# Optimization experiments

Measured on AMD Instinct MI355X. Metric: run time of the kernel, lower is better.

Reference implementation:

```python
import jax, jax.numpy as jnp
import numpy as np

A = -0.75  # torch bicubic coefficient
SCALES = [1.0, 0.9, 0.8, 0.7, 0.6]  # level=5
SOFTMAX_SCALE = 10.0
RES_SCALE = 1.0
ESCAPE_NAN = 1e-4


def _cubic_w(d):
    d = jnp.abs(d)
    return jnp.where(d <= 1.0, ((A + 2.0) * d - (A + 3.0)) * d * d + 1.0,
                     jnp.where(d < 2.0, ((A * d - 5.0 * A) * d + 8.0 * A) * d - 4.0 * A, 0.0))


def _resize_axis(x, out_size, axis):
    # bicubic, align_corners=True, 4-tap cubic conv with border clamp (matches torch)
    in_size = x.shape[axis]
    src = jnp.arange(out_size, dtype=jnp.float32) * (float(in_size - 1) / float(out_size - 1))
    i0 = jnp.floor(src).astype(jnp.int32)
    frac = src - i0.astype(jnp.float32)
    idx = jnp.clip(jnp.stack([i0 - 1, i0, i0 + 1, i0 + 2], 0), 0, in_size - 1)  # [4,out]
    w = jnp.stack([_cubic_w(frac + 1.0), _cubic_w(frac), _cubic_w(1.0 - frac), _cubic_w(2.0 - frac)], 0)  # [4,out]
    xm = jnp.moveaxis(x, axis, 0)
    g = xm[idx]  # [4,out,...]
    out = jnp.einsum('ko...,ko->o...', g, w)
    return jnp.moveaxis(out, 0, axis)


def bicubic_resize(x, oh, ow):
    return _resize_axis(_resize_axis(x, oh, 2), ow, 3)


def prelu(x, a):
    return jnp.where(x >= 0, x, a * x)


def conv1x1(x, W, b):
    # x [B,C,H,W], W [O,C], b [O]
    return jnp.einsum('oc,bchw->bohw', W, x) + b[None, :, None, None]


def extract_patches(x):
    # x [B,C,H,W] -> [B, H*W, C, 3, 3], 'same' padding, stride 1 (torch unfold order C,kh,kw)
    B, C, H, Wd = x.shape
    xp = jnp.pad(x, ((0, 0), (0, 0), (1, 1), (1, 1)))
    sl = [xp[:, :, dy:dy + H, dx:dx + Wd] for dy in range(3) for dx in range(3)]
    p = jnp.stack(sl, 0).reshape(3, 3, B, C, H, Wd)
    p = jnp.transpose(p, (2, 4, 5, 3, 0, 1))  # [B,H,W,C,3,3]
    return p.reshape(B, H * Wd, C, 3, 3)


def setup_inputs() -> dict:
    key = jax.random.key(0)
    ks = jax.random.split(key, 8)
    B, C, H, Wd = 2, 64, 64, 64
    Cm = 32
    return {
        'input': jax.random.normal(ks[0], (B, C, H, Wd), jnp.float32),
        'input_ref': jax.random.normal(ks[1], (B, C, H, Wd), jnp.float32),
        'Wb': jax.random.normal(ks[2], (Cm, C), jnp.float32) * 0.1,
        'bb': jax.random.normal(ks[3], (Cm,), jnp.float32) * 0.01,
        'Wm': jax.random.normal(ks[4], (Cm, C), jnp.float32) * 0.1,
        'bm': jax.random.normal(ks[5], (Cm,), jnp.float32) * 0.01,
        'Wa': jax.random.normal(ks[6], (C, C), jnp.float32) * 0.1,
        'ba': jax.random.normal(ks[7], (C,), jnp.float32) * 0.01,
        'a_prelu': jnp.full((1,), 0.25, jnp.float32),
    }


def reference(input, input_ref, Wb, bb, Wm, bm, Wa, ba, a_prelu):
    B, C, H, Wd = input.shape
    a = a_prelu[0]
    match_base = prelu(conv1x1(input, Wb, bb), a)  # [B,Cm,H,W]

    w_list, rw_list = [], []
    for s in SCALES:
        ref = input_ref if s == 1.0 else bicubic_resize(input_ref, int(H * s), int(Wd * s))
        base = prelu(conv1x1(ref, Wa, ba), a)   # conv_assembly
        rw_list.append(extract_patches(base))   # [B,Li,C,3,3]
        m = prelu(conv1x1(ref, Wm, bm), a)      # conv_match
        w_list.append(extract_patches(m))       # [B,Li,Cm,3,3]
    w = jnp.concatenate(w_list, axis=1)    # [B,L,Cm,3,3]
    rw = jnp.concatenate(rw_list, axis=1)  # [B,L,C,3,3]

    dn = ('NCHW', 'OIHW', 'NCHW')

    def per_sample(xi, wi, rwi):
        # xi [Cm,H,W]; wi [L,Cm,3,3]; rwi [L,C,3,3]
        nrm = jnp.maximum(jnp.sqrt(jnp.sum(wi * wi, axis=(1, 2, 3), keepdims=True)), ESCAPE_NAN)
        wn = wi / nrm
        scores = jax.lax.conv_general_dilated(xi[None], wn, (1, 1), [(1, 1), (1, 1)], dimension_numbers=dn)[0]  # [L,H,W]
        yi = jax.nn.softmax(scores * SOFTMAX_SCALE, axis=0)
        # conv_transpose2d(yi, rwi, stride=1, padding=1) == conv2d with flipped, transposed kernel, pad 1
        k = jnp.transpose(rwi, (1, 0, 2, 3))[:, :, ::-1, ::-1]  # [C,L,3,3]
        out = jax.lax.conv_general_dilated(yi[None], k, (1, 1), [(1, 1), (1, 1)], dimension_numbers=dn)[0] / 4.0
        return out  # [C,H,W]

    y = jax.vmap(per_sample)(match_base, w, rw)
    return y + input * RES_SCALE
```

## Files before the change

### kernel.cpp

```cpp
#include <hip/hip_runtime.h>
#include <stdint.h>


typedef __attribute__((ext_vector_type(8))) short bf16x8;
typedef __attribute__((ext_vector_type(4))) float f32x4;
typedef unsigned short ushort_t;

#define L_TOT  13326
#define NCHT   417
#define NPIX   4096
#define BCHUNK_E 9216
#define RCHUNK_E 18432
#define LOG2E10 14.4269504f
#define CT 256

__device__ __forceinline__ float cubw(float d) {
  d = fabsf(d);
  if (d <= 1.f) return (1.25f * d - 2.25f) * d * d + 1.f;
  if (d < 2.f)  return ((-0.75f * d + 3.75f) * d - 6.f) * d + 3.f;
  return 0.f;
}

__device__ __forceinline__ void decode_l(int l, int& S, int& off) {
  if (l < 4096)       { S = 64; off = 0; }
  else if (l < 7345)  { S = 57; off = 4096; }
  else if (l < 9946)  { S = 51; off = 7345; }
  else if (l < 11882) { S = 44; off = 9946; }
  else                { S = 38; off = 11882; }
}

__device__ __forceinline__ ushort_t f2bf(float f) {
  union { float f; uint32_t u; } v; v.f = f;
  uint32_t r = (v.u + 0x7fffu + ((v.u >> 16) & 1u)) >> 16;
  return (ushort_t)r;
}

__device__ __forceinline__ float preluf(float x, float a) { return x >= 0.f ? x : a * x; }

__device__ __forceinline__ void gll16(const ushort_t* g, ushort_t* l) {
  __builtin_amdgcn_global_load_lds(
      (const __attribute__((address_space(1))) unsigned int*)g,
      (__attribute__((address_space(3))) unsigned int*)l, 16, 0, 0);
}

__global__ void k_convref(const float* __restrict__ inref,
                          const float* __restrict__ Wm, const float* __restrict__ bm,
                          const float* __restrict__ Wa, const float* __restrict__ ba,
                          const float* __restrict__ ap,
                          float* __restrict__ mref, float* __restrict__ aref) {
  __shared__ float T[64][CT];
  __shared__ float Wy[CT][5], Wx[CT][5];
  __shared__ int   IY[CT], IX[CT];
  int blk = blockIdx.x;
  int oh = blk & 1; int lt = (blk >> 1) % 53; int b = blk / 106;
  int l0 = lt * CT;
  int tid = threadIdx.x;
  float a = ap[0];
  {
    int gl = l0 + tid;
    if (gl < L_TOT) {
      int S, off; decode_l(gl, S, off);
      int li = gl - off; int ly = li / S, lx = li % S;
      if (S == 64) {
        IY[tid] = -1; IX[tid] = ly * 64 + lx;
      } else {
        float sc = (float)(63.0 / (double)(S - 1));
        float sy = (float)ly * sc, sx = (float)lx * sc;
        int iy = (int)floorf(sy), ix = (int)floorf(sx);
        float fy = sy - (float)iy, fx = sx - (float)ix;
        IY[tid] = iy; IX[tid] = ix;
        Wy[tid][0] = cubw(fy + 1.f); Wy[tid][1] = cubw(fy);
        Wy[tid][2] = cubw(1.f - fy); Wy[tid][3] = cubw(2.f - fy);
        Wx[tid][0] = cubw(fx + 1.f); Wx[tid][1] = cubw(fx);
        Wx[tid][2] = cubw(1.f - fx); Wx[tid][3] = cubw(2.f - fx);
      }
    }
  }
  __syncthreads();
  for (int i = tid; i < 64 * CT; i += 256) {
    int c = i >> 8; int l2 = i & 255;
    int gl = l0 + l2;
    float val = 0.f;
    if (gl < L_TOT) {
      const float* img = inref + (size_t)(b * 64 + c) * 4096;
      int iy = IY[l2];
      if (iy == -1) {
        val = img[IX[l2]];
      } else {
        int ix = IX[l2];
        #pragma unroll
        for (int t = 0; t < 4; ++t) {
          int ty = iy - 1 + t; ty = ty < 0 ? 0 : (ty > 63 ? 63 : ty);
          float rv = 0.f;
          #pragma unroll
          for (int u = 0; u < 4; ++u) {
            int tx = ix - 1 + u; tx = tx < 0 ? 0 : (tx > 63 ? 63 : tx);
            rv += Wx[l2][u] * img[ty * 64 + tx];
          }
          val += Wy[l2][t] * rv;
        }
      }
    }
    T[c][l2] = val;
  }
  __syncthreads();
  int gl = l0 + tid;
  if (gl >= L_TOT) return;
  for (int oc = oh * 48; oc < oh * 48 + 48; ++oc) {
    const float* Wrow; float s;
    if (oc < 32) { Wrow = Wm + oc * 64; s = bm[oc]; }
    else         { Wrow = Wa + (oc - 32) * 64; s = ba[oc - 32]; }
    #pragma unroll 8
    for (int c = 0; c < 64; ++c) s += Wrow[c] * T[c][tid];
    s = preluf(s, a);
    if (oc < 32) mref[(size_t)(b * 32 + oc) * L_TOT + gl] = s;
    else         aref[(size_t)(b * 64 + oc - 32) * L_TOT + gl] = s;
  }
}

__global__ void k_mb(const float* __restrict__ input, const float* __restrict__ Wb,
                     const float* __restrict__ bb, const float* __restrict__ ap,
                     float* __restrict__ mbb, int n) {
  int idx = blockIdx.x * 256 + threadIdx.x;
  if (idx >= n) return;
  int p = idx % NPIX; int cm = (idx / NPIX) % 32; int b = idx / (32 * NPIX);
  float a = ap[0];
  float acc = bb[cm];
  for (int c = 0; c < 64; ++c) acc += Wb[cm * 64 + c] * input[(size_t)(b * 64 + c) * NPIX + p];
  mbb[(size_t)(b * 32 + cm) * NPIX + p] = preluf(acc, a);
}

__global__ void k_stage1(const float* __restrict__ mref, const float* __restrict__ mbb,
                         float* __restrict__ ssq, float* __restrict__ ssqA, int n) {
  int idx = blockIdx.x * 256 + threadIdx.x;
  if (idx >= n) return;
  if (idx < 2 * L_TOT) {
    int l = idx % L_TOT; int b = idx / L_TOT;
    float s = 0.f;
    for (int c = 0; c < 32; ++c) { float v = mref[(size_t)(b * 32 + c) * L_TOT + l]; s += v * v; }
    ssq[idx] = s;
  } else {
    int j = idx - 2 * L_TOT;
    int p = j % NPIX; int b = j / NPIX;
    float s = 0.f;
    for (int c = 0; c < 32; ++c) { float v = mbb[(size_t)(b * 32 + c) * NPIX + p]; s += v * v; }
    ssqA[j] = s;
  }
}

__global__ void k_stage2(const float* __restrict__ ssq, const float* __restrict__ ssqA,
                         float* __restrict__ invn, float* __restrict__ Mlog, int n) {
  int idx = blockIdx.x * 256 + threadIdx.x;
  if (idx >= n) return;
  if (idx < 2 * L_TOT) {
    int l = idx % L_TOT; int b = idx / L_TOT;
    int S, off; decode_l(l, S, off);
    int li = l - off; int ly = li / S, lx = li % S;
    float acc = 0.f;
    for (int dy = -1; dy <= 1; ++dy) {
      int ny = ly + dy; if (ny < 0 || ny >= S) continue;
      for (int dx = -1; dx <= 1; ++dx) {
        int nx = lx + dx; if (nx < 0 || nx >= S) continue;
        acc += ssq[(size_t)b * L_TOT + off + ny * S + nx];
      }
    }
    float nrm = sqrtf(acc); nrm = fmaxf(nrm, 1e-4f);
    invn[idx] = 1.f / nrm;
  } else {
    int j = idx - 2 * L_TOT;
    int p = j % NPIX; int b = j / NPIX;
    int y = p / 64, x = p % 64;
    float acc = 0.f;
    for (int dy = -1; dy <= 1; ++dy) {
      int ny = y + dy; if (ny < 0 || ny >= 64) continue;
      for (int dx = -1; dx <= 1; ++dx) {
        int nx = x + dx; if (nx < 0 || nx >= 64) continue;
        acc += ssqA[(size_t)b * NPIX + ny * 64 + nx];
      }
    }
    float qn = sqrtf(acc);
    float m = fmaxf(0.7f * qn, qn - 7.f);
    Mlog[j] = LOG2E10 * m;
  }
}

#define N_BS (2 * NCHT * 1152)
#define N_AIM (2 * NPIX * 36)
#define N_RS (2 * NCHT * 576 * 4)
__global__ void k_pack(const float* __restrict__ mref, const float* __restrict__ invn,
                       const float* __restrict__ mbb, const float* __restrict__ aref,
                       ushort_t* __restrict__ Bs, ushort_t* __restrict__ Am,
                       ushort_t* __restrict__ Rs, int n) {
  int idx = blockIdx.x * 256 + threadIdx.x;
  if (idx >= n) return;
  ushort_t v[8];
  if (idx < N_BS) {
    int segp = idx % 36; int col = (idx / 36) % 32;
    int ch = (idx / 1152) % NCHT; int b = idx / (1152 * NCHT);
    int segl = (segp & ~3) | ((segp & 3) ^ ((col >> 1) & 3));
    int l = ch * 32 + col;
    if (l < L_TOT) {
      int S, off; decode_l(l, S, off);
      int li = l - off; int ly = li / S, lx = li % S;
      float iv = invn[(size_t)b * L_TOT + l];
      #pragma unroll
      for (int e = 0; e < 8; ++e) {
        int k = segl * 8 + e;
        int c = k / 9; int r = k % 9; int dy = r / 3 - 1, dx = r % 3 - 1;
        int ny = ly + dy, nx = lx + dx;
        float val = 0.f;
        if (ny >= 0 && ny < S && nx >= 0 && nx < S)
          val = mref[(size_t)(b * 32 + c) * L_TOT + off + ny * S + nx] * iv;
        v[e] = f2bf(val);
      }
    } else {
      #pragma unroll
      for (int e = 0; e < 8; ++e) v[e] = 0;
    }
    *(uint4*)(Bs + ((size_t)(b * NCHT + ch) * BCHUNK_E + col * 288 + segp * 8)) = *(const uint4*)v;
  } else if (idx < N_BS + N_AIM) {
    int j = idx - N_BS;
    int k8 = j % 36; int p = (j / 36) % NPIX; int b = j / (36 * NPIX);
    int y = p / 64, x = p % 64;
    #pragma unroll
    for (int e = 0; e < 8; ++e) {
      int k = k8 * 8 + e;
      int c = k / 9; int r = k % 9; int dy = r / 3 - 1, dx = r % 3 - 1;
      int ny = y + dy, nx = x + dx;
      float val = 0.f;
      if (ny >= 0 && ny < 64 && nx >= 0 && nx < 64)
        val = mbb[(size_t)(b * 32 + c) * NPIX + ny * 64 + nx];
      v[e] = f2bf(val);
    }
    *(uint4*)(Am + ((size_t)(b * NPIX + p) * 288 + k8 * 8)) = *(const uint4*)v;
  } else {
    int j = idx - N_BS - N_AIM;
    int phys = j & 3; int q = j >> 2;
    int col = q % 576; q /= 576;
    int ch = q % NCHT; int b = q / NCHT;
    int c = col / 9; int r = col % 9; int dy = r / 3 - 1, dx = r % 3 - 1;
    int seg = phys ^ ((col >> 1) & 3);
    int lbase = ch * 32 + seg * 8;
    #pragma unroll
    for (int e = 0; e < 8; ++e) {
      int l = lbase + e;
      float val = 0.f;
      if (l < L_TOT) {
        int S, off; decode_l(l, S, off);
        int li = l - off; int ly = li / S, lx = li % S;
        int ny = ly + dy, nx = lx + dx;
        if (ny >= 0 && ny < S && nx >= 0 && nx < S)
          val = aref[(size_t)(b * 64 + c) * L_TOT + off + ny * S + nx];
      }
      v[e] = f2bf(val);
    }
    *(uint4*)(Rs + ((size_t)(b * NCHT + ch) * RCHUNK_E + col * 32 + phys * 8)) = *(const uint4*)v;
  }
}

__global__ __launch_bounds__(512, 2) void k_attn(const ushort_t* __restrict__ Am,
                                                 const ushort_t* __restrict__ Bs,
                                                 const ushort_t* __restrict__ Rs,
                                                 const float* __restrict__ Mlog,
                                                 float* __restrict__ Og,
                                                 float* __restrict__ Ol) {
  __shared__ ushort_t Rl[3][RCHUNK_E];
  __shared__ ushort_t Bl[2][BCHUNK_E];
  __shared__ ushort_t Pl[2][2048];
  int tid = threadIdx.x;
  int xcd = blockIdx.x & 7; int slot = blockIdx.x >> 3;
  int group = xcd >> 1;
  int spl = group & 1; int b = group >> 1;
  int tile = slot * 2 + (xcd & 1);
  int p0 = tile * 64;
  int wave = tid >> 6, lane = tid & 63, quad = lane >> 4, ln = lane & 15;
  int rbS = wave & 3, cbh = wave >> 2;
  int g = wave & 3, zrh = wave >> 2;
  int c0 = spl ? 209 : 0, c1 = spl ? NCHT : 209;

  bf16x8 af[9];
  {
    const ushort_t* arow = Am + (size_t)(b * NPIX + p0 + rbS * 16 + ln) * 288;
    #pragma unroll
    for (int kk = 0; kk < 9; ++kk) af[kk] = *(const bf16x8*)(arow + kk * 32 + quad * 8);
  }
  float mlg[4];
  #pragma unroll
  for (int r = 0; r < 4; ++r)
    mlg[r] = Mlog[(size_t)b * NPIX + p0 + rbS * 16 + quad * 4 + r];

  f32x4 acc[2][9];
  #pragma unroll
  for (int h = 0; h < 2; ++h)
    #pragma unroll
    for (int t = 0; t < 9; ++t) { acc[h][t][0] = acc[h][t][1] = acc[h][t][2] = acc[h][t][3] = 0.f; }
  float psum[4] = {0.f, 0.f, 0.f, 0.f};

  const ushort_t* RsB = Rs + (size_t)b * NCHT * RCHUNK_E + lane * 8;
  const ushort_t* BsB = Bs + (size_t)b * NCHT * BCHUNK_E + lane * 8;

  {
    const ushort_t* sB0 = BsB + (size_t)c0 * BCHUNK_E;
    ushort_t* dB0 = Bl[c0 & 1];
    #pragma unroll
    for (int u = wave; u < 18; u += 8) gll16(sB0 + u * 512, dB0 + u * 512);
    const ushort_t* sB1 = BsB + (size_t)(c0 + 1) * BCHUNK_E;
    ushort_t* dB1 = Bl[(c0 + 1) & 1];
    #pragma unroll
    for (int u = wave; u < 18; u += 8) gll16(sB1 + u * 512, dB1 + u * 512);
    const ushort_t* sR = RsB + (size_t)c0 * RCHUNK_E;
    ushort_t* dR = Rl[c0 % 3];
    #pragma unroll
    for (int u = wave; u < 36; u += 8) gll16(sR + u * 512, dR + u * 512);
  }
  __syncthreads();

  int col32 = cbh * 16 + ln;
  int bswz = (col32 >> 1) & 3;
  int rpar = c0 % 3;
  for (int ch = c0; ch < c1; ++ch) {
    int par = ch & 1;
    int rnext = rpar == 2 ? 0 : rpar + 1;
    f32x4 sa, sb;
    sa[0] = sa[1] = sa[2] = sa[3] = 0.f;
    sb[0] = sb[1] = sb[2] = sb[3] = 0.f;
    #pragma unroll
    for (int kk = 0; kk < 9; ++kk) {
      int segp = kk * 4 + (quad ^ bswz);
      bf16x8 bf = *(const bf16x8*)&Bl[par][col32 * 288 + segp * 8];
      if (kk == 4 || kk == 5 || kk == 6 || kk == 7)
        sb = __builtin_amdgcn_mfma_f32_16x16x32_bf16(af[kk], bf, sb, 0, 0, 0);
      else
        sa = __builtin_amdgcn_mfma_f32_16x16x32_bf16(af[kk], bf, sa, 0, 0, 0);
    }
    int colw = ch * 32 + col32;
    bool valid = colw < L_TOT;
    #pragma unroll
    for (int r = 0; r < 4; ++r) {
      float sv = sa[r] + sb[r];
      float pv = valid ? exp2f(fmaf(sv, LOG2E10, -mlg[r])) : 0.f;
      int row = rbS * 16 + quad * 4 + r;
      int seg = cbh * 2 + (ln >> 3);
      int swz = seg ^ ((row >> 1) & 3);
      Pl[par][row * 32 + swz * 8 + (ln & 7)] = f2bf(pv);
      psum[r] += pv;
    }
    __syncthreads();
    if (ch + 2 < c1) {
      const ushort_t* sB = BsB + (size_t)(ch + 2) * BCHUNK_E;
      ushort_t* dB = Bl[par];
      #pragma unroll
      for (int u = wave; u < 18; u += 8) gll16(sB + u * 512, dB + u * 512);
    }
    if (ch + 1 < c1) {
      const ushort_t* sR = RsB + (size_t)(ch + 1) * RCHUNK_E;
      ushort_t* dR = Rl[rnext];
      #pragma unroll
      for (int u = wave; u < 36; u += 8) gll16(sR + u * 512, dR + u * 512);
    }
    bf16x8 pf0, pf1;
    {
      int sw = quad ^ ((ln >> 1) & 3);
      pf0 = *(const bf16x8*)&Pl[par][(zrh * 32 + ln) * 32 + sw * 8];
      pf1 = *(const bf16x8*)&Pl[par][(zrh * 32 + 16 + ln) * 32 + sw * 8];
    }
    #pragma unroll
    for (int t = 0; t < 9; ++t) {
      int col = g * 144 + t * 16 + ln;
      int swz = quad ^ ((col >> 1) & 3);
      bf16x8 rf = *(const bf16x8*)&Rl[rpar][col * 32 + swz * 8];
      acc[0][t] = __builtin_amdgcn_mfma_f32_16x16x32_bf16(pf0, rf, acc[0][t], 0, 0, 0);
      acc[1][t] = __builtin_amdgcn_mfma_f32_16x16x32_bf16(pf1, rf, acc[1][t], 0, 0, 0);
    }
    rpar = rnext;
  }

  #pragma unroll
  for (int m = 1; m <= 8; m <<= 1)
    #pragma unroll
    for (int r = 0; r < 4; ++r) psum[r] += __shfl_xor(psum[r], m);
  int sb2 = spl * 2 + b;
  if (ln == 0) {
    #pragma unroll
    for (int r = 0; r < 4; ++r) {
      int row = p0 + rbS * 16 + quad * 4 + r;
      Ol[(size_t)(sb2 * 2 + cbh) * NPIX + row] = psum[r];
    }
  }
  #pragma unroll
  for (int h = 0; h < 2; ++h)
    #pragma unroll
    for (int t = 0; t < 9; ++t) {
      int colg = g * 144 + t * 16 + ln;
      #pragma unroll
      for (int r = 0; r < 4; ++r) {
        int row = p0 + zrh * 32 + h * 16 + quad * 4 + r;
        Og[((size_t)sb2 * NPIX + row) * 576 + colg] = acc[h][t][r];
      }
    }
}

__global__ void k_inv(const float* __restrict__ Ol, float* __restrict__ inv, int n) {
  int idx = blockIdx.x * 256 + threadIdx.x;
  if (idx >= n) return;
  int b = idx / NPIX; int p = idx % NPIX;
  float s = 0.f;
  #pragma unroll
  for (int spl = 0; spl < 2; ++spl)
    #pragma unroll
    for (int cbh = 0; cbh < 2; ++cbh)
      s += Ol[(size_t)(((spl * 2 + b) * 2) + cbh) * NPIX + p];
  inv[idx] = 1.f / s;
}

__global__ void k_final(const float* __restrict__ Og, const float* __restrict__ inv,
                        const float* __restrict__ input, float* __restrict__ out) {
  __shared__ float T[32][65];
  int blk = blockIdx.x;
  int xh = blk & 1; int y = (blk >> 1) & 63; int b = blk >> 7;
  int tid = threadIdx.x;
  const size_t S1 = (size_t)2 * NPIX * 576;
  for (int it = 0; it < 8; ++it) {
    int lin = it * 256 + tid;
    int c = lin & 63, x32 = lin >> 6;
    int x = xh * 32 + x32;
    float acc = 0.f;
    for (int j = 0; j < 3; ++j) {
      int qy = y + 1 - j; if (qy < 0 || qy >= 64) continue;
      for (int i2 = 0; i2 < 3; ++i2) {
        int qx = x + 1 - i2; if (qx < 0 || qx >= 64) continue;
        int p = qy * 64 + qx;
        size_t e = ((size_t)b * NPIX + p) * 576 + c * 9 + j * 3 + i2;
        acc += (Og[e] + Og[e + S1]) * inv[b * NPIX + p];
      }
    }
    T[x32][c] = acc;
  }
  __syncthreads();
  for (int it = 0; it < 8; ++it) {
    int lin = it * 256 + tid;
    int x32 = lin & 31, c = lin >> 5;
    int o = ((b * 64 + c) * 64 + y) * 64 + xh * 32 + x32;
    out[o] = 0.25f * T[x32][c] + input[o];
  }
}

extern "C" void kernel_launch(void* const* d_in, const int* in_sizes, int n_in,
                              void* d_out, int out_size, void* d_ws, size_t ws_size,
                              hipStream_t stream) {
  (void)in_sizes; (void)n_in; (void)out_size; (void)ws_size;
  const float* input = (const float*)d_in[0];
  const float* inref = (const float*)d_in[1];
  const float* Wb = (const float*)d_in[2];
  const float* bb = (const float*)d_in[3];
  const float* Wm = (const float*)d_in[4];
  const float* bm = (const float*)d_in[5];
  const float* Wa = (const float*)d_in[6];
  const float* ba = (const float*)d_in[7];
  const float* ap = (const float*)d_in[8];
  float* out = (float*)d_out;

  char* ws = (char*)d_ws;
  size_t off = 0;
  auto alloc = [&](size_t bytes) -> char* {
    char* p = ws + off; off = (off + bytes + 255) & ~(size_t)255; return p;
  };
  ushort_t* Am   = (ushort_t*)alloc((size_t)2 * NPIX * 288 * 2);
  ushort_t* Bs   = (ushort_t*)alloc((size_t)2 * NCHT * BCHUNK_E * 2);
  ushort_t* Rs   = (ushort_t*)alloc((size_t)2 * NCHT * RCHUNK_E * 2);
  float*    Ol   = (float*)alloc((size_t)8 * NPIX * 4);
  float*    inv  = (float*)alloc((size_t)2 * NPIX * 4);
  float*    Mlog = (float*)alloc((size_t)2 * NPIX * 4);
  float*    ssqA = (float*)alloc((size_t)2 * NPIX * 4);
  size_t og_bytes = (size_t)4 * NPIX * 576 * 4;
  char* big = alloc(og_bytes);
  float* Og = (float*)big;
  size_t eoff = 0;
  auto ealloc = [&](size_t bytes) -> char* {
    char* p = big + eoff; eoff = (eoff + bytes + 255) & ~(size_t)255; return p;
  };
  float* mref = (float*)ealloc((size_t)2 * 32 * L_TOT * 4);
  float* aref = (float*)ealloc((size_t)2 * 64 * L_TOT * 4);
  float* mbb  = (float*)ealloc((size_t)2 * 32 * NPIX * 4);
  float* ssq  = (float*)ealloc((size_t)2 * L_TOT * 4);
  float* invn = (float*)ealloc((size_t)2 * L_TOT * 4);

  k_convref<<<212, 256, 0, stream>>>(inref, Wm, bm, Wa, ba, ap, mref, aref);
  int n3 = 2 * 32 * NPIX;
  k_mb<<<(n3 + 255) / 256, 256, 0, stream>>>(input, Wb, bb, ap, mbb, n3);
  int ns = 2 * L_TOT + 2 * NPIX;
  k_stage1<<<(ns + 255) / 256, 256, 0, stream>>>(mref, mbb, ssq, ssqA, ns);
  k_stage2<<<(ns + 255) / 256, 256, 0, stream>>>(ssq, ssqA, invn, Mlog, ns);
  int np = N_BS + N_AIM + N_RS;
  k_pack<<<(np + 255) / 256, 256, 0, stream>>>(mref, invn, mbb, aref, Bs, Am, Rs, np);

  k_attn<<<256, 512, 0, stream>>>(Am, Bs, Rs, Mlog, Og, Ol);
  k_inv<<<(2 * NPIX + 255) / 256, 256, 0, stream>>>(Ol, inv, 2 * NPIX);
  k_final<<<256, 256, 0, stream>>>(Og, inv, input, out);
}
```

Measured before the change: 470.4 us.

## Specialize waves into score/softmax producers and PV consumers pipelined by chunk

The attention kernel now splits its eight waves into two roles. Waves 0-3 compute the QK scores and exp-probabilities for chunk ch, each covering two 16-row tiles. Waves 4-7 run the P·R MFMA accumulation for chunk ch-1, each covering all 64 rows, with the accumulator and the A fragments sharing one register array. This lets the softmax/exp phase of one chunk overlap the value accumulation of the previous chunk, and the R staging drops from three LDS buffers to two. The risks are load imbalance between the two roles, high register use per wave, and fewer waves available to hide latency in each phase.

```diff
diff --git a/kernel.cpp b/kernel.cpp
--- a/kernel.cpp
+++ b/kernel.cpp
@@ -264,7 +264,7 @@
                                                  const float* __restrict__ Mlog,
                                                  float* __restrict__ Og,
                                                  float* __restrict__ Ol) {
-  __shared__ ushort_t Rl[3][RCHUNK_E];
+  __shared__ ushort_t Rl[2][RCHUNK_E];
   __shared__ ushort_t Bl[2][BCHUNK_E];
   __shared__ ushort_t Pl[2][2048];
   int tid = threadIdx.x;
@@ -274,130 +274,140 @@
   int tile = slot * 2 + (xcd & 1);
   int p0 = tile * 64;
   int wave = tid >> 6, lane = tid & 63, quad = lane >> 4, ln = lane & 15;
-  int rbS = wave & 3, cbh = wave >> 2;
-  int g = wave & 3, zrh = wave >> 2;
+  bool isS = wave < 4;
+  int rbp = wave & 1, cbh = (wave >> 1) & 1;
+  int g = wave & 3;
   int c0 = spl ? 209 : 0, c1 = spl ? NCHT : 209;
 
-  bf16x8 af[9];
-  {
-    const ushort_t* arow = Am + (size_t)(b * NPIX + p0 + rbS * 16 + ln) * 288;
-    #pragma unroll
-    for (int kk = 0; kk < 9; ++kk) af[kk] = *(const bf16x8*)(arow + kk * 32 + quad * 8);
-  }
-  float mlg[4];
-  #pragma unroll
-  for (int r = 0; r < 4; ++r)
-    mlg[r] = Mlog[(size_t)b * NPIX + p0 + rbS * 16 + quad * 4 + r];
-
-  f32x4 acc[2][9];
-  #pragma unroll
-  for (int h = 0; h < 2; ++h)
-    #pragma unroll
-    for (int t = 0; t < 9; ++t) { acc[h][t][0] = acc[h][t][1] = acc[h][t][2] = acc[h][t][3] = 0.f; }
-  float psum[4] = {0.f, 0.f, 0.f, 0.f};
+  f32x4 st[36];
+  float mlg[2][4], psum[2][4];
+
+  if (isS) {
+    #pragma unroll
+    for (int h = 0; h < 2; ++h) {
+      const ushort_t* arow = Am + (size_t)(b * NPIX + p0 + (rbp + 2 * h) * 16 + ln) * 288;
+      #pragma unroll
+      for (int kk = 0; kk < 9; ++kk)
+        st[h * 9 + kk] = __builtin_bit_cast(f32x4, *(const bf16x8*)(arow + kk * 32 + quad * 8));
+      #pragma unroll
+      for (int r = 0; r < 4; ++r) {
+        mlg[h][r] = Mlog[(size_t)b * NPIX + p0 + (rbp + 2 * h) * 16 + quad * 4 + r];
+        psum[h][r] = 0.f;
+      }
+    }
+  } else {
+    #pragma unroll
+    for (int i = 0; i < 36; ++i) { st[i][0] = 0.f; st[i][1] = 0.f; st[i][2] = 0.f; st[i][3] = 0.f; }
+  }
 
   const ushort_t* RsB = Rs + (size_t)b * NCHT * RCHUNK_E + lane * 8;
   const ushort_t* BsB = Bs + (size_t)b * NCHT * BCHUNK_E + lane * 8;
 
-  {
-    const ushort_t* sB0 = BsB + (size_t)c0 * BCHUNK_E;
-    ushort_t* dB0 = Bl[c0 & 1];
-    #pragma unroll
-    for (int u = wave; u < 18; u += 8) gll16(sB0 + u * 512, dB0 + u * 512);
-    const ushort_t* sB1 = BsB + (size_t)(c0 + 1) * BCHUNK_E;
-    ushort_t* dB1 = Bl[(c0 + 1) & 1];
-    #pragma unroll
-    for (int u = wave; u < 18; u += 8) gll16(sB1 + u * 512, dB1 + u * 512);
-    const ushort_t* sR = RsB + (size_t)c0 * RCHUNK_E;
-    ushort_t* dR = Rl[c0 % 3];
-    #pragma unroll
-    for (int u = wave; u < 36; u += 8) gll16(sR + u * 512, dR + u * 512);
-  }
-  __syncthreads();
+  auto stageB = [&](int chunk, int sl) {
+    const ushort_t* s = BsB + (size_t)chunk * BCHUNK_E;
+    ushort_t* d = Bl[sl];
+    #pragma unroll
+    for (int u = wave; u < 18; u += 8) gll16(s + u * 512, d + u * 512);
+  };
+  auto stageR = [&](int chunk, int sl) {
+    const ushort_t* s = RsB + (size_t)chunk * RCHUNK_E;
+    ushort_t* d = Rl[sl];
+    #pragma unroll
+    for (int u = wave; u < 36; u += 8) gll16(s + u * 512, d + u * 512);
+  };
 
   int col32 = cbh * 16 + ln;
   int bswz = (col32 >> 1) & 3;
-  int rpar = c0 % 3;
-  for (int ch = c0; ch < c1; ++ch) {
-    int par = ch & 1;
-    int rnext = rpar == 2 ? 0 : rpar + 1;
-    f32x4 sa, sb;
-    sa[0] = sa[1] = sa[2] = sa[3] = 0.f;
-    sb[0] = sb[1] = sb[2] = sb[3] = 0.f;
-    #pragma unroll
-    for (int kk = 0; kk < 9; ++kk) {
-      int segp = kk * 4 + (quad ^ bswz);
-      bf16x8 bf = *(const bf16x8*)&Bl[par][col32 * 288 + segp * 8];
-      if (kk == 4 || kk == 5 || kk == 6 || kk == 7)
-        sb = __builtin_amdgcn_mfma_f32_16x16x32_bf16(af[kk], bf, sb, 0, 0, 0);
-      else
-        sa = __builtin_amdgcn_mfma_f32_16x16x32_bf16(af[kk], bf, sa, 0, 0, 0);
-    }
-    int colw = ch * 32 + col32;
-    bool valid = colw < L_TOT;
-    #pragma unroll
-    for (int r = 0; r < 4; ++r) {
-      float sv = sa[r] + sb[r];
-      float pv = valid ? exp2f(fmaf(sv, LOG2E10, -mlg[r])) : 0.f;
-      int row = rbS * 16 + quad * 4 + r;
-      int seg = cbh * 2 + (ln >> 3);
-      int swz = seg ^ ((row >> 1) & 3);
-      Pl[par][row * 32 + swz * 8 + (ln & 7)] = f2bf(pv);
-      psum[r] += pv;
-    }
-    __syncthreads();
-    if (ch + 2 < c1) {
-      const ushort_t* sB = BsB + (size_t)(ch + 2) * BCHUNK_E;
-      ushort_t* dB = Bl[par];
-      #pragma unroll
-      for (int u = wave; u < 18; u += 8) gll16(sB + u * 512, dB + u * 512);
-    }
-    if (ch + 1 < c1) {
-      const ushort_t* sR = RsB + (size_t)(ch + 1) * RCHUNK_E;
-      ushort_t* dR = Rl[rnext];
-      #pragma unroll
-      for (int u = wave; u < 36; u += 8) gll16(sR + u * 512, dR + u * 512);
-    }
-    bf16x8 pf0, pf1;
-    {
-      int sw = quad ^ ((ln >> 1) & 3);
-      pf0 = *(const bf16x8*)&Pl[par][(zrh * 32 + ln) * 32 + sw * 8];
-      pf1 = *(const bf16x8*)&Pl[par][(zrh * 32 + 16 + ln) * 32 + sw * 8];
-    }
+  int psw = quad ^ ((ln >> 1) & 3);
+
+  auto zstep = [&](int parz) {
+    bf16x8 pf[4];
+    #pragma unroll
+    for (int j = 0; j < 4; ++j)
+      pf[j] = *(const bf16x8*)&Pl[parz][(j * 16 + ln) * 32 + psw * 8];
     #pragma unroll
     for (int t = 0; t < 9; ++t) {
       int col = g * 144 + t * 16 + ln;
       int swz = quad ^ ((col >> 1) & 3);
-      bf16x8 rf = *(const bf16x8*)&Rl[rpar][col * 32 + swz * 8];
-      acc[0][t] = __builtin_amdgcn_mfma_f32_16x16x32_bf16(pf0, rf, acc[0][t], 0, 0, 0);
-      acc[1][t] = __builtin_amdgcn_mfma_f32_16x16x32_bf16(pf1, rf, acc[1][t], 0, 0, 0);
-    }
-    rpar = rnext;
-  }
-
-  #pragma unroll
-  for (int m = 1; m <= 8; m <<= 1)
-    #pragma unroll
-    for (int r = 0; r < 4; ++r) psum[r] += __shfl_xor(psum[r], m);
-  int sb2 = spl * 2 + b;
-  if (ln == 0) {
-    #pragma unroll
-    for (int r = 0; r < 4; ++r) {
-      int row = p0 + rbS * 16 + quad * 4 + r;
-      Ol[(size_t)(sb2 * 2 + cbh) * NPIX + row] = psum[r];
-    }
-  }
-  #pragma unroll
-  for (int h = 0; h < 2; ++h)
-    #pragma unroll
-    for (int t = 0; t < 9; ++t) {
-      int colg = g * 144 + t * 16 + ln;
-      #pragma unroll
-      for (int r = 0; r < 4; ++r) {
-        int row = p0 + zrh * 32 + h * 16 + quad * 4 + r;
-        Og[((size_t)sb2 * NPIX + row) * 576 + colg] = acc[h][t][r];
-      }
-    }
+      bf16x8 rf = *(const bf16x8*)&Rl[parz][col * 32 + swz * 8];
+      #pragma unroll
+      for (int j = 0; j < 4; ++j)
+        st[j * 9 + t] = __builtin_amdgcn_mfma_f32_16x16x32_bf16(pf[j], rf, st[j * 9 + t], 0, 0, 0);
+    }
+  };
+
+  stageB(c0, c0 & 1);
+  stageB(c0 + 1, (c0 + 1) & 1);
+  stageR(c0, c0 & 1);
+  __syncthreads();
+
+  for (int ch = c0; ch < c1; ++ch) {
+    int par = ch & 1;
+    if (isS) {
+      f32x4 s0, s1;
+      s0[0] = s0[1] = s0[2] = s0[3] = 0.f;
+      s1[0] = s1[1] = s1[2] = s1[3] = 0.f;
+      #pragma unroll
+      for (int kk = 0; kk < 9; ++kk) {
+        int segp = kk * 4 + (quad ^ bswz);
+        bf16x8 bfrag = *(const bf16x8*)&Bl[par][col32 * 288 + segp * 8];
+        s0 = __builtin_amdgcn_mfma_f32_16x16x32_bf16(__builtin_bit_cast(bf16x8, st[kk]), bfrag, s0, 0, 0, 0);
+        s1 = __builtin_amdgcn_mfma_f32_16x16x32_bf16(__builtin_bit_cast(bf16x8, st[9 + kk]), bfrag, s1, 0, 0, 0);
+      }
+      int colw = ch * 32 + col32;
+      bool valid = colw < L_TOT;
+      #pragma unroll
+      for (int h = 0; h < 2; ++h)
+        #pragma unroll
+        for (int r = 0; r < 4; ++r) {
+          float sv = h ? s1[r] : s0[r];
+          float pv = valid ? exp2f(fmaf(sv, LOG2E10, -mlg[h][r])) : 0.f;
+          int row = (rbp + 2 * h) * 16 + quad * 4 + r;
+          int seg = cbh * 2 + (ln >> 3);
+          int swz = seg ^ ((row >> 1) & 3);
+          Pl[par][row * 32 + swz * 8 + (ln & 7)] = f2bf(pv);
+          psum[h][r] += pv;
+        }
+    } else if (ch > c0) {
+      zstep(par ^ 1);
+    }
+    __syncthreads();
+    if (ch + 2 < c1) stageB(ch + 2, par);
+    if (ch + 1 < c1) stageR(ch + 1, par ^ 1);
+  }
+
+  if (isS) {
+    #pragma unroll
+    for (int m = 1; m <= 8; m <<= 1)
+      #pragma unroll
+      for (int h = 0; h < 2; ++h)
+        #pragma unroll
+        for (int r = 0; r < 4; ++r) psum[h][r] += __shfl_xor(psum[h][r], m);
+    int sb2 = spl * 2 + b;
+    if (ln == 0) {
+      #pragma unroll
+      for (int h = 0; h < 2; ++h)
+        #pragma unroll
+        for (int r = 0; r < 4; ++r) {
+          int row = p0 + (rbp + 2 * h) * 16 + quad * 4 + r;
+          Ol[(size_t)(sb2 * 2 + cbh) * NPIX + row] = psum[h][r];
+        }
+    }
+  } else {
+    zstep((c1 - 1) & 1);
+    int sb2 = spl * 2 + b;
+    #pragma unroll
+    for (int j = 0; j < 4; ++j)
+      #pragma unroll
+      for (int t = 0; t < 9; ++t) {
+        int colg = g * 144 + t * 16 + ln;
+        #pragma unroll
+        for (int r = 0; r < 4; ++r) {
+          int row = p0 + j * 16 + quad * 4 + r;
+          Og[((size_t)sb2 * NPIX + row) * 576 + colg] = st[j * 9 + t][r];
+        }
+      }
+  }
 }
 
 __global__ void k_inv(const float* __restrict__ Ol, float* __restrict__ inv, int n) {
```

New measurement: 500.5 us. 1.06x slower.

## Software-pipeline score and aggregation MFMAs across chunks with partial vmcnt waits

Applied to the files above, without the earlier changes.

Restructures the main chunk loop so the score MFMAs for chunk ch are interleaved with the aggregation MFMAs for chunk ch-1, using a prologue and an epilogue. Full __syncthreads is replaced by an s_waitcnt vmcnt(4) plus s_barrier, so in-flight prefetches of the next chunk are not drained at every iteration. R is now staged two chunks ahead in its triple buffer. The intent is to overlap the exp/softmax dependency chain and the global loads with MFMA work and to remove a barrier per chunk. The hand-counted vmcnt value is fragile if the number of loads issued per wave changes.

```diff
diff --git a/kernel.cpp b/kernel.cpp
--- a/kernel.cpp
+++ b/kernel.cpp
@@ -299,39 +299,44 @@
   const ushort_t* RsB = Rs + (size_t)b * NCHT * RCHUNK_E + lane * 8;
   const ushort_t* BsB = Bs + (size_t)b * NCHT * BCHUNK_E + lane * 8;
 
-  {
-    const ushort_t* sB0 = BsB + (size_t)c0 * BCHUNK_E;
-    ushort_t* dB0 = Bl[c0 & 1];
-    #pragma unroll
-    for (int u = wave; u < 18; u += 8) gll16(sB0 + u * 512, dB0 + u * 512);
-    const ushort_t* sB1 = BsB + (size_t)(c0 + 1) * BCHUNK_E;
-    ushort_t* dB1 = Bl[(c0 + 1) & 1];
-    #pragma unroll
-    for (int u = wave; u < 18; u += 8) gll16(sB1 + u * 512, dB1 + u * 512);
-    const ushort_t* sR = RsB + (size_t)c0 * RCHUNK_E;
-    ushort_t* dR = Rl[c0 % 3];
-    #pragma unroll
-    for (int u = wave; u < 36; u += 8) gll16(sR + u * 512, dR + u * 512);
-  }
-  __syncthreads();
+  auto stageB = [&](int chunk, int sl) {
+    const ushort_t* s = BsB + (size_t)chunk * BCHUNK_E;
+    ushort_t* d = Bl[sl];
+    #pragma unroll
+    for (int u = wave; u < 18; u += 8) gll16(s + u * 512, d + u * 512);
+  };
+  auto stageR = [&](int chunk, int sl) {
+    const ushort_t* s = RsB + (size_t)chunk * RCHUNK_E;
+    ushort_t* d = Rl[sl];
+    #pragma unroll
+    for (int u = wave; u < 36; u += 8) gll16(s + u * 512, d + u * 512);
+  };
 
   int col32 = cbh * 16 + ln;
   int bswz = (col32 >> 1) & 3;
-  int rpar = c0 % 3;
-  for (int ch = c0; ch < c1; ++ch) {
-    int par = ch & 1;
-    int rnext = rpar == 2 ? 0 : rpar + 1;
+  int psw = quad ^ ((ln >> 1) & 3);
+
+  stageB(c0, c0 & 1);
+  stageB(c0 + 1, (c0 + 1) & 1);
+  stageR(c0, c0 % 3);
+  stageR(c0 + 1, (c0 + 1) % 3);
+  __syncthreads();
+
+  int rz = c0 % 3;
+
+  {
+    int ch = c0, par = ch & 1;
     f32x4 sa, sb;
     sa[0] = sa[1] = sa[2] = sa[3] = 0.f;
     sb[0] = sb[1] = sb[2] = sb[3] = 0.f;
     #pragma unroll
     for (int kk = 0; kk < 9; ++kk) {
       int segp = kk * 4 + (quad ^ bswz);
-      bf16x8 bf = *(const bf16x8*)&Bl[par][col32 * 288 + segp * 8];
-      if (kk == 4 || kk == 5 || kk == 6 || kk == 7)
-        sb = __builtin_amdgcn_mfma_f32_16x16x32_bf16(af[kk], bf, sb, 0, 0, 0);
+      bf16x8 bfrag = *(const bf16x8*)&Bl[par][col32 * 288 + segp * 8];
+      if (kk >= 4 && kk <= 7)
+        sb = __builtin_amdgcn_mfma_f32_16x16x32_bf16(af[kk], bfrag, sb, 0, 0, 0);
       else
-        sa = __builtin_amdgcn_mfma_f32_16x16x32_bf16(af[kk], bf, sa, 0, 0, 0);
+        sa = __builtin_amdgcn_mfma_f32_16x16x32_bf16(af[kk], bfrag, sa, 0, 0, 0);
     }
     int colw = ch * 32 + col32;
     bool valid = colw < L_TOT;
@@ -345,34 +350,69 @@
       Pl[par][row * 32 + swz * 8 + (ln & 7)] = f2bf(pv);
       psum[r] += pv;
     }
-    __syncthreads();
+    asm volatile("s_waitcnt vmcnt(4) lgkmcnt(0)\n\ts_barrier" ::: "memory");
     if (ch + 2 < c1) {
-      const ushort_t* sB = BsB + (size_t)(ch + 2) * BCHUNK_E;
-      ushort_t* dB = Bl[par];
-      #pragma unroll
-      for (int u = wave; u < 18; u += 8) gll16(sB + u * 512, dB + u * 512);
-    }
-    if (ch + 1 < c1) {
-      const ushort_t* sR = RsB + (size_t)(ch + 1) * RCHUNK_E;
-      ushort_t* dR = Rl[rnext];
-      #pragma unroll
-      for (int u = wave; u < 36; u += 8) gll16(sR + u * 512, dR + u * 512);
-    }
-    bf16x8 pf0, pf1;
-    {
-      int sw = quad ^ ((ln >> 1) & 3);
-      pf0 = *(const bf16x8*)&Pl[par][(zrh * 32 + ln) * 32 + sw * 8];
-      pf1 = *(const bf16x8*)&Pl[par][(zrh * 32 + 16 + ln) * 32 + sw * 8];
-    }
+      stageB(ch + 2, par);
+      int s2 = rz + 2; if (s2 >= 3) s2 -= 3;
+      stageR(ch + 2, s2);
+    }
+  }
+
+  for (int ch = c0 + 1; ch < c1; ++ch) {
+    int par = ch & 1;
+    bf16x8 pf0 = *(const bf16x8*)&Pl[par ^ 1][(zrh * 32 + ln) * 32 + psw * 8];
+    bf16x8 pf1 = *(const bf16x8*)&Pl[par ^ 1][(zrh * 32 + 16 + ln) * 32 + psw * 8];
+    f32x4 sa, sb;
+    sa[0] = sa[1] = sa[2] = sa[3] = 0.f;
+    sb[0] = sb[1] = sb[2] = sb[3] = 0.f;
+    #pragma unroll
+    for (int kk = 0; kk < 9; ++kk) {
+      int segp = kk * 4 + (quad ^ bswz);
+      bf16x8 bfrag = *(const bf16x8*)&Bl[par][col32 * 288 + segp * 8];
+      if (kk >= 4 && kk <= 7)
+        sb = __builtin_amdgcn_mfma_f32_16x16x32_bf16(af[kk], bfrag, sb, 0, 0, 0);
+      else
+        sa = __builtin_amdgcn_mfma_f32_16x16x32_bf16(af[kk], bfrag, sa, 0, 0, 0);
+      int col = g * 144 + kk * 16 + ln;
+      int swz = quad ^ ((col >> 1) & 3);
+      bf16x8 rf = *(const bf16x8*)&Rl[rz][col * 32 + swz * 8];
+      acc[0][kk] = __builtin_amdgcn_mfma_f32_16x16x32_bf16(pf0, rf, acc[0][kk], 0, 0, 0);
+      acc[1][kk] = __builtin_amdgcn_mfma_f32_16x16x32_bf16(pf1, rf, acc[1][kk], 0, 0, 0);
+    }
+    int colw = ch * 32 + col32;
+    bool valid = colw < L_TOT;
+    #pragma unroll
+    for (int r = 0; r < 4; ++r) {
+      float sv = sa[r] + sb[r];
+      float pv = valid ? exp2f(fmaf(sv, LOG2E10, -mlg[r])) : 0.f;
+      int row = rbS * 16 + quad * 4 + r;
+      int seg = cbh * 2 + (ln >> 3);
+      int swz = seg ^ ((row >> 1) & 3);
+      Pl[par][row * 32 + swz * 8 + (ln & 7)] = f2bf(pv);
+      psum[r] += pv;
+    }
+    asm volatile("s_waitcnt vmcnt(4) lgkmcnt(0)\n\ts_barrier" ::: "memory");
+    if (ch + 2 < c1) {
+      stageB(ch + 2, par);
+      stageR(ch + 2, rz);
+    }
+    rz = rz == 2 ? 0 : rz + 1;
+  }
+
+  asm volatile("s_waitcnt vmcnt(0)\n\ts_barrier" ::: "memory");
+
+  {
+    int parz = (c1 - 1) & 1;
+    bf16x8 pf0 = *(const bf16x8*)&Pl[parz][(zrh * 32 + ln) * 32 + psw * 8];
+    bf16x8 pf1 = *(const bf16x8*)&Pl[parz][(zrh * 32 + 16 + ln) * 32 + psw * 8];
     #pragma unroll
     for (int t = 0; t < 9; ++t) {
       int col = g * 144 + t * 16 + ln;
       int swz = quad ^ ((col >> 1) & 3);
-      bf16x8 rf = *(const bf16x8*)&Rl[rpar][col * 32 + swz * 8];
+      bf16x8 rf = *(const bf16x8*)&Rl[rz][col * 32 + swz * 8];
       acc[0][t] = __builtin_amdgcn_mfma_f32_16x16x32_bf16(pf0, rf, acc[0][t], 0, 0, 0);
       acc[1][t] = __builtin_amdgcn_mfma_f32_16x16x32_bf16(pf1, rf, acc[1][t], 0, 0, 0);
     }
-    rpar = rnext;
   }
 
   #pragma unroll
```

Result: slower. 512.8 us (+9.0%).

## Add 128-row attention tile variant with four-way key split

Applied to the files above, without the earlier changes.

Adds k_attn128, which processes 128 query pixels per block instead of 64, splitting the key chunks four ways across XCD groups rather than two. Each staged B/R chunk in shared memory is reused by twice as many query rows, which halves global and LDS traffic per FLOP. R staging drops from triple to double buffering to fit LDS. The cost is more accumulator registers, a larger partial-output buffer, and more partial sums for k_final to reduce. The new path is chosen at runtime only if the workspace is large enough, otherwise the old kernel runs.

```diff
diff --git a/kernel.cpp b/kernel.cpp
--- a/kernel.cpp
+++ b/kernel.cpp
@@ -258,12 +258,12 @@
   }
 }
 
-__global__ __launch_bounds__(512, 2) void k_attn(const ushort_t* __restrict__ Am,
-                                                 const ushort_t* __restrict__ Bs,
-                                                 const ushort_t* __restrict__ Rs,
-                                                 const float* __restrict__ Mlog,
-                                                 float* __restrict__ Og,
-                                                 float* __restrict__ Ol) {
+__global__ __launch_bounds__(512, 2) void k_attn64(const ushort_t* __restrict__ Am,
+                                                   const ushort_t* __restrict__ Bs,
+                                                   const ushort_t* __restrict__ Rs,
+                                                   const float* __restrict__ Mlog,
+                                                   float* __restrict__ Og,
+                                                   float* __restrict__ Ol) {
   __shared__ ushort_t Rl[3][RCHUNK_E];
   __shared__ ushort_t Bl[2][BCHUNK_E];
   __shared__ ushort_t Pl[2][2048];
@@ -400,13 +400,148 @@
     }
 }
 
-__global__ void k_inv(const float* __restrict__ Ol, float* __restrict__ inv, int n) {
+__global__ __launch_bounds__(512, 2) void k_attn128(const ushort_t* __restrict__ Am,
+                                                    const ushort_t* __restrict__ Bs,
+                                                    const ushort_t* __restrict__ Rs,
+                                                    const float* __restrict__ Mlog,
+                                                    float* __restrict__ Og,
+                                                    float* __restrict__ Ol) {
+  __shared__ ushort_t Rl[2][RCHUNK_E];
+  __shared__ ushort_t Bl[2][BCHUNK_E];
+  __shared__ ushort_t Pl[2][4096];
+  int tid = threadIdx.x;
+  int xcd = blockIdx.x & 7; int slot = blockIdx.x >> 3;
+  int spl = xcd >> 1; int b = xcd & 1;
+  int p0 = slot * 128;
+  int wave = tid >> 6, lane = tid & 63, quad = lane >> 4, ln = lane & 15;
+  int rbq = wave & 3, cb = wave >> 2;
+  int g = wave & 3, zrh = wave >> 2;
+  int c0 = (spl * NCHT) >> 2;
+  int c1 = ((spl + 1) * NCHT) >> 2;
+
+  bf16x8 af[2][9];
+  float mlg[2][4], psum[2][4];
+  #pragma unroll
+  for (int h = 0; h < 2; ++h) {
+    const ushort_t* arow = Am + (size_t)(b * NPIX + p0 + (rbq + 4 * h) * 16 + ln) * 288;
+    #pragma unroll
+    for (int kk = 0; kk < 9; ++kk) af[h][kk] = *(const bf16x8*)(arow + kk * 32 + quad * 8);
+    #pragma unroll
+    for (int r = 0; r < 4; ++r) {
+      mlg[h][r] = Mlog[(size_t)b * NPIX + p0 + (rbq + 4 * h) * 16 + quad * 4 + r];
+      psum[h][r] = 0.f;
+    }
+  }
+  f32x4 acc[4][9];
+  #pragma unroll
+  for (int j = 0; j < 4; ++j)
+    #pragma unroll
+    for (int t = 0; t < 9; ++t) { acc[j][t][0] = acc[j][t][1] = acc[j][t][2] = acc[j][t][3] = 0.f; }
+
+  const ushort_t* RsB = Rs + (size_t)b * NCHT * RCHUNK_E + lane * 8;
+  const ushort_t* BsB = Bs + (size_t)b * NCHT * BCHUNK_E + lane * 8;
+
+  auto stageB = [&](int chunk, int sl) {
+    const ushort_t* s = BsB + (size_t)chunk * BCHUNK_E;
+    ushort_t* d = Bl[sl];
+    #pragma unroll
+    for (int u = wave; u < 18; u += 8) gll16(s + u * 512, d + u * 512);
+  };
+  auto stageR = [&](int chunk, int sl) {
+    const ushort_t* s = RsB + (size_t)chunk * RCHUNK_E;
+    ushort_t* d = Rl[sl];
+    #pragma unroll
+    for (int u = wave; u < 36; u += 8) gll16(s + u * 512, d + u * 512);
+  };
+
+  int col32 = cb * 16 + ln;
+  int bswz = (col32 >> 1) & 3;
+  int psw = quad ^ ((ln >> 1) & 3);
+
+  stageB(c0, c0 & 1);
+  stageB(c0 + 1, (c0 + 1) & 1);
+  stageR(c0, c0 & 1);
+  __syncthreads();
+
+  for (int ch = c0; ch < c1; ++ch) {
+    int par = ch & 1;
+    f32x4 s0, s1;
+    s0[0] = s0[1] = s0[2] = s0[3] = 0.f;
+    s1[0] = s1[1] = s1[2] = s1[3] = 0.f;
+    #pragma unroll
+    for (int kk = 0; kk < 9; ++kk) {
+      int segp = kk * 4 + (quad ^ bswz);
+      bf16x8 bfrag = *(const bf16x8*)&Bl[par][col32 * 288 + segp * 8];
+      s0 = __builtin_amdgcn_mfma_f32_16x16x32_bf16(af[0][kk], bfrag, s0, 0, 0, 0);
+      s1 = __builtin_amdgcn_mfma_f32_16x16x32_bf16(af[1][kk], bfrag, s1, 0, 0, 0);
+    }
+    int colw = ch * 32 + col32;
+    bool valid = colw < L_TOT;
+    #pragma unroll
+    for (int h = 0; h < 2; ++h)
+      #pragma unroll
+      for (int r = 0; r < 4; ++r) {
+        float sv = h ? s1[r] : s0[r];
+        float pv = valid ? exp2f(fmaf(sv, LOG2E10, -mlg[h][r])) : 0.f;
+        int row = (rbq + 4 * h) * 16 + quad * 4 + r;
+        int seg = cb * 2 + (ln >> 3);
+        int swz = seg ^ ((row >> 1) & 3);
+        Pl[par][row * 32 + swz * 8 + (ln & 7)] = f2bf(pv);
+        psum[h][r] += pv;
+      }
+    __syncthreads();
+    if (ch + 2 < c1) stageB(ch + 2, par);
+    if (ch + 1 < c1) stageR(ch + 1, par ^ 1);
+    bf16x8 pf[4];
+    #pragma unroll
+    for (int j = 0; j < 4; ++j)
+      pf[j] = *(const bf16x8*)&Pl[par][(zrh * 64 + j * 16 + ln) * 32 + psw * 8];
+    #pragma unroll
+    for (int t = 0; t < 9; ++t) {
+      int col = g * 144 + t * 16 + ln;
+      int swz = quad ^ ((col >> 1) & 3);
+      bf16x8 rf = *(const bf16x8*)&Rl[par][col * 32 + swz * 8];
+      #pragma unroll
+      for (int j = 0; j < 4; ++j)
+        acc[j][t] = __builtin_amdgcn_mfma_f32_16x16x32_bf16(pf[j], rf, acc[j][t], 0, 0, 0);
+    }
+  }
+
+  #pragma unroll
+  for (int m = 1; m <= 8; m <<= 1)
+    #pragma unroll
+    for (int h = 0; h < 2; ++h)
+      #pragma unroll
+      for (int r = 0; r < 4; ++r) psum[h][r] += __shfl_xor(psum[h][r], m);
+  int sb2 = spl * 2 + b;
+  if (ln == 0) {
+    #pragma unroll
+    for (int h = 0; h < 2; ++h)
+      #pragma unroll
+      for (int r = 0; r < 4; ++r) {
+        int row = p0 + (rbq + 4 * h) * 16 + quad * 4 + r;
+        Ol[(size_t)(sb2 * 2 + cb) * NPIX + row] = psum[h][r];
+      }
+  }
+  #pragma unroll
+  for (int j = 0; j < 4; ++j)
+    #pragma unroll
+    for (int t = 0; t < 9; ++t) {
+      int colg = g * 144 + t * 16 + ln;
+      #pragma unroll
+      for (int r = 0; r < 4; ++r) {
+        int row = p0 + zrh * 64 + j * 16 + quad * 4 + r;
+        Og[((size_t)sb2 * NPIX + row) * 576 + colg] = acc[j][t][r];
+      }
+    }
+}
+
+__global__ void k_inv(const float* __restrict__ Ol, float* __restrict__ inv, int n, int nspl) {
   int idx = blockIdx.x * 256 + threadIdx.x;
   if (idx >= n) return;
   int b = idx / NPIX; int p = idx % NPIX;
   float s = 0.f;
-  #pragma unroll
-  for (int spl = 0; spl < 2; ++spl)
+  for (int spl = 0; spl < nspl; ++spl)
     #pragma unroll
     for (int cbh = 0; cbh < 2; ++cbh)
       s += Ol[(size_t)(((spl * 2 + b) * 2) + cbh) * NPIX + p];
@@ -414,7 +549,7 @@
 }
 
 __global__ void k_final(const float* __restrict__ Og, const float* __restrict__ inv,
-                        const float* __restrict__ input, float* __restrict__ out) {
+                        const float* __restrict__ input, float* __restrict__ out, int nsl) {
   __shared__ float T[32][65];
   int blk = blockIdx.x;
   int xh = blk & 1; int y = (blk >> 1) & 63; int b = blk >> 7;
@@ -431,7 +566,9 @@
         int qx = x + 1 - i2; if (qx < 0 || qx >= 64) continue;
         int p = qy * 64 + qx;
         size_t e = ((size_t)b * NPIX + p) * 576 + c * 9 + j * 3 + i2;
-        acc += (Og[e] + Og[e + S1]) * inv[b * NPIX + p];
+        float tap = 0.f;
+        for (int s = 0; s < nsl; ++s) tap += Og[e + (size_t)s * S1];
+        acc += tap * inv[b * NPIX + p];
       }
     }
     T[x32][c] = acc;
@@ -448,7 +585,7 @@
 extern "C" void kernel_launch(void* const* d_in, const int* in_sizes, int n_in,
                               void* d_out, int out_size, void* d_ws, size_t ws_size,
                               hipStream_t stream) {
-  (void)in_sizes; (void)n_in; (void)out_size; (void)ws_size;
+  (void)in_sizes; (void)n_in; (void)out_size;
   const float* input = (const float*)d_in[0];
   const float* inref = (const float*)d_in[1];
   const float* Wb = (const float*)d_in[2];
@@ -468,12 +605,14 @@
   ushort_t* Am   = (ushort_t*)alloc((size_t)2 * NPIX * 288 * 2);
   ushort_t* Bs   = (ushort_t*)alloc((size_t)2 * NCHT * BCHUNK_E * 2);
   ushort_t* Rs   = (ushort_t*)alloc((size_t)2 * NCHT * RCHUNK_E * 2);
-  float*    Ol   = (float*)alloc((size_t)8 * NPIX * 4);
+  float*    Ol   = (float*)alloc((size_t)16 * NPIX * 4);
   float*    inv  = (float*)alloc((size_t)2 * NPIX * 4);
   float*    Mlog = (float*)alloc((size_t)2 * NPIX * 4);
   float*    ssqA = (float*)alloc((size_t)2 * NPIX * 4);
-  size_t og_bytes = (size_t)4 * NPIX * 576 * 4;
-  char* big = alloc(og_bytes);
+  size_t og64  = (size_t)4 * NPIX * 576 * 4;
+  size_t og128 = og64 * 2;
+  bool use128 = (off + og128 + 512) <= ws_size;
+  char* big = alloc(use128 ? og128 : og64);
   float* Og = (float*)big;
   size_t eoff = 0;
   auto ealloc = [&](size_t bytes) -> char* {
@@ -494,7 +633,13 @@
   int np = N_BS + N_AIM + N_RS;
   k_pack<<<(np + 255) / 256, 256, 0, stream>>>(mref, invn, mbb, aref, Bs, Am, Rs, np);
 
-  k_attn<<<256, 512, 0, stream>>>(Am, Bs, Rs, Mlog, Og, Ol);
-  k_inv<<<(2 * NPIX + 255) / 256, 256, 0, stream>>>(Ol, inv, 2 * NPIX);
-  k_final<<<256, 256, 0, stream>>>(Og, inv, input, out);
-}
+  if (use128) {
+    k_attn128<<<256, 512, 0, stream>>>(Am, Bs, Rs, Mlog, Og, Ol);
+    k_inv<<<(2 * NPIX + 255) / 256, 256, 0, stream>>>(Ol, inv, 2 * NPIX, 4);
+    k_final<<<256, 256, 0, stream>>>(Og, inv, input, out, 4);
+  } else {
+    k_attn64<<<256, 512, 0, stream>>>(Am, Bs, Rs, Mlog, Og, Ol);
+    k_inv<<<(2 * NPIX + 255) / 256, 256, 0, stream>>>(Ol, inv, 2 * NPIX, 2);
+    k_final<<<256, 256, 0, stream>>>(Og, inv, input, out, 2);
+  }
+}
```

Measured after the change: 619.3 us. 31.6% more time.
